# Optimization experiments

Hardware: AMD Instinct MI355X
Metric: run time of the kernel (lower is better)

Reference implementation:

```python
import jax, jax.numpy as jnp
import numpy as np
import math

B, S, HID, NH = 2, 2048, 1024, 16
HD = HID // NH  # head_dim = 64
TEMPERATURE = 1.0


def setup_inputs() -> dict:
    key = jax.random.key(0)
    ks = jax.random.split(key, 6)
    w = lambda k: (jax.random.normal(k, (HID, HID), dtype=jnp.float32) * 0.02)
    return {
        "hidden_states": jax.random.normal(ks[0], (B, S, HID), dtype=jnp.float32),
        "attention_mask": jnp.ones((B, S), dtype=jnp.float32),
        "Wq": w(ks[1]), "bq": jnp.zeros((HID,), jnp.float32),
        "Wk": w(ks[2]), "bk": jnp.zeros((HID,), jnp.float32),
        "Wv": w(ks[3]), "bv": jnp.zeros((HID,), jnp.float32),
        "Wo": w(ks[4]), "bo": jnp.zeros((HID,), jnp.float32),
    }


def reference(hidden_states, attention_mask, Wq, bq, Wk, bk, Wv, bv, Wo, bo):
    b, s, hid = hidden_states.shape
    heads = lambda x: x.reshape(b, s, NH, HD).transpose(0, 2, 1, 3)  # [b,h,s,d]

    q = heads(hidden_states @ Wq.T + bq)
    k = heads(hidden_states @ Wk.T + bk)
    v = heads(hidden_states @ Wv.T + bv)

    # padding mask applied multiplicatively to k and v
    m = attention_mask[:, None, :, None]  # [b,1,s,1]
    k = k * m
    v = v * m

    # auxiliary Hopfield state: k^T @ v per head -> [b,h,d,d]
    state = jnp.einsum("bhsd,bhse->bhde", k, v)

    # energy / scores
    energy = jnp.einsum("bhqd,bhkd->bhqk", q, k) / (TEMPERATURE * math.sqrt(HD))
    causal = jnp.triu(jnp.ones((s, s), dtype=bool), k=1)  # True above diagonal
    energy = jnp.where(causal[None, None], -jnp.inf, energy)
    energy = jnp.where(attention_mask[:, None, None, :] == 0, -jnp.inf, energy)

    attn = jax.nn.softmax(energy, axis=-1)
    out = jnp.einsum("bhqk,bhkd->bhqd", attn, v)
    out = out.transpose(0, 2, 1, 3).reshape(b, s, hid)
    out = out @ Wo.T + bo
    return out, state
```

## Files before the change

kernel.cpp:

```cpp
#include <hip/hip_runtime.h>
#include <hip/hip_bf16.h>

#define B_ 2
#define S_ 2048
#define HID_ 1024
#define NH_ 16
#define HD_ 64
#define MTOK (B_*S_)
#define LDQKV 3072

typedef __attribute__((ext_vector_type(8))) __bf16 bf16x8;
typedef __attribute__((ext_vector_type(4))) __bf16 bf16x4;
typedef __attribute__((ext_vector_type(4))) float f32x4;

__device__ __forceinline__ void gl16(__bf16* lds, const __bf16* g) {
  __builtin_amdgcn_global_load_lds(
      (const __attribute__((address_space(1))) void*)g,
      (__attribute__((address_space(3))) void*)lds, 16, 0, 0);
}
__device__ __forceinline__ void gl4(float* lds, const float* g) {
  __builtin_amdgcn_global_load_lds(
      (const __attribute__((address_space(1))) void*)g,
      (__attribute__((address_space(3))) void*)lds, 4, 0, 0);
}

__global__ __launch_bounds__(256) void cast_all(
    const float* __restrict__ X,
    const float* __restrict__ Wq, const float* __restrict__ Wk,
    const float* __restrict__ Wv, const float* __restrict__ Wo,
    __bf16* __restrict__ Xb, __bf16* __restrict__ Wqkvb, __bf16* __restrict__ Wob)
{
  int i = blockIdx.x * 256 + threadIdx.x;
  const float* src; __bf16* dst; int j;
  if (i < (1 << 20))              { src = X;  dst = Xb;                 j = i; }
  else if (i < (1<<20)+(1<<18))   { src = Wq; dst = Wqkvb;              j = i - (1<<20); }
  else if (i < (1<<20)+(2<<18))   { src = Wk; dst = Wqkvb + (1<<20);    j = i - (1<<20) - (1<<18); }
  else if (i < (1<<20)+(3<<18))   { src = Wv; dst = Wqkvb + (2<<20);    j = i - (1<<20) - (2<<18); }
  else                            { src = Wo; dst = Wob;                j = i - (1<<20) - (3<<18); }
  float4 v = reinterpret_cast<const float4*>(src)[j];
  bf16x4 o;
  o[0] = (__bf16)v.x; o[1] = (__bf16)v.y; o[2] = (__bf16)v.z; o[3] = (__bf16)v.w;
  reinterpret_cast<bf16x4*>(dst)[j] = o;
}

__global__ __launch_bounds__(256) void gemm_qkv(
    const __bf16* __restrict__ A, const __bf16* __restrict__ W,
    const float* __restrict__ bq, const float* __restrict__ bk,
    const float* __restrict__ bv, const float* __restrict__ mask,
    __bf16* __restrict__ C)
{
  __shared__ __bf16 As[2][128 * 32];
  __shared__ __bf16 Bs[2][128 * 32];
  const int t = threadIdx.x;
  const int m0 = blockIdx.y * 128;
  const int n0 = blockIdx.x * 128;
  const int lane = t & 63;
  const int w = t >> 6;
  const int wr = (w >> 1) * 64;
  const int wc = (w & 1) * 64;
  const int fr = lane & 15;
  const int kg = lane >> 4;

  f32x4 acc[4][4];
  #pragma unroll
  for (int i = 0; i < 4; i++)
    #pragma unroll
    for (int j = 0; j < 4; j++) acc[i][j] = (f32x4)0.f;

  const int srow = w * 16 + (lane >> 2);
  const int scol = (lane & 3) * 8;
  const __bf16* ap0 = A + (size_t)(m0 + srow) * HID_ + scol;
  const __bf16* ap1 = A + (size_t)(m0 + 64 + srow) * HID_ + scol;
  const __bf16* wp0 = W + (size_t)(n0 + srow) * HID_ + scol;
  const __bf16* wp1 = W + (size_t)(n0 + 64 + srow) * HID_ + scol;

  #define GSTAGE(buf, koff) \
    gl16(&As[buf][w * 512], ap0 + (koff)); \
    gl16(&As[buf][2048 + w * 512], ap1 + (koff)); \
    gl16(&Bs[buf][w * 512], wp0 + (koff)); \
    gl16(&Bs[buf][2048 + w * 512], wp1 + (koff));

  GSTAGE(0, 0);
  for (int k0 = 0; k0 < HID_; k0 += 32) {
    const int cur = (k0 >> 5) & 1;
    if (k0 + 32 < HID_) {
      GSTAGE(cur ^ 1, k0 + 32);
      asm volatile("s_waitcnt vmcnt(4)" ::: "memory");
    } else {
      asm volatile("s_waitcnt vmcnt(0)" ::: "memory");
    }
    __builtin_amdgcn_sched_barrier(0);
    __builtin_amdgcn_s_barrier();
    bf16x8 af[4], bf[4];
    #pragma unroll
    for (int m = 0; m < 4; m++) af[m] = *(const bf16x8*)&As[cur][(wr + m*16 + fr) * 32 + kg*8];
    #pragma unroll
    for (int n = 0; n < 4; n++) bf[n] = *(const bf16x8*)&Bs[cur][(wc + n*16 + fr) * 32 + kg*8];
    #pragma unroll
    for (int m = 0; m < 4; m++)
      #pragma unroll
      for (int n = 0; n < 4; n++)
        acc[m][n] = __builtin_amdgcn_mfma_f32_16x16x32_bf16(af[m], bf[n], acc[m][n], 0, 0, 0);
    __builtin_amdgcn_s_barrier();
  }

  const int region = n0 >> 10;
  const float* bias = region == 0 ? bq : (region == 1 ? bk : bv);
  const int nloc = n0 & 1023;

  #pragma unroll
  for (int m = 0; m < 4; m++) {
    #pragma unroll
    for (int r = 0; r < 4; r++) {
      int row = m0 + wr + m*16 + kg*4 + r;
      float rs = region ? mask[row] : 1.f;
      #pragma unroll
      for (int n = 0; n < 4; n++) {
        int c = wc + n*16 + fr;
        float v = (acc[m][n][r] + bias[nloc + c]) * rs;
        C[(size_t)row * LDQKV + n0 + c] = (__bf16)v;
      }
    }
  }
}

__global__ __launch_bounds__(256) void gemm_o(
    const __bf16* __restrict__ A, const __bf16* __restrict__ W,
    const float* __restrict__ bias, float* __restrict__ C)
{
  __shared__ __bf16 As[2][128 * 32];
  __shared__ __bf16 Bs[2][128 * 32];
  const int t = threadIdx.x;
  const int m0 = blockIdx.y * 128;
  const int n0 = blockIdx.x * 128;
  const int lane = t & 63;
  const int w = t >> 6;
  const int wr = (w >> 1) * 64;
  const int wc = (w & 1) * 64;
  const int fr = lane & 15;
  const int kg = lane >> 4;

  f32x4 acc[4][4];
  #pragma unroll
  for (int i = 0; i < 4; i++)
    #pragma unroll
    for (int j = 0; j < 4; j++) acc[i][j] = (f32x4)0.f;

  const int srow = w * 16 + (lane >> 2);
  const int scol = (lane & 3) * 8;
  const __bf16* ap0 = A + (size_t)(m0 + srow) * HID_ + scol;
  const __bf16* ap1 = A + (size_t)(m0 + 64 + srow) * HID_ + scol;
  const __bf16* wp0 = W + (size_t)(n0 + srow) * HID_ + scol;
  const __bf16* wp1 = W + (size_t)(n0 + 64 + srow) * HID_ + scol;

  GSTAGE(0, 0);
  for (int k0 = 0; k0 < HID_; k0 += 32) {
    const int cur = (k0 >> 5) & 1;
    if (k0 + 32 < HID_) {
      GSTAGE(cur ^ 1, k0 + 32);
      asm volatile("s_waitcnt vmcnt(4)" ::: "memory");
    } else {
      asm volatile("s_waitcnt vmcnt(0)" ::: "memory");
    }
    __builtin_amdgcn_sched_barrier(0);
    __builtin_amdgcn_s_barrier();
    bf16x8 af[4], bf[4];
    #pragma unroll
    for (int m = 0; m < 4; m++) af[m] = *(const bf16x8*)&As[cur][(wr + m*16 + fr) * 32 + kg*8];
    #pragma unroll
    for (int n = 0; n < 4; n++) bf[n] = *(const bf16x8*)&Bs[cur][(wc + n*16 + fr) * 32 + kg*8];
    #pragma unroll
    for (int m = 0; m < 4; m++)
      #pragma unroll
      for (int n = 0; n < 4; n++)
        acc[m][n] = __builtin_amdgcn_mfma_f32_16x16x32_bf16(af[m], bf[n], acc[m][n], 0, 0, 0);
    __builtin_amdgcn_s_barrier();
  }

  #pragma unroll
  for (int m = 0; m < 4; m++) {
    #pragma unroll
    for (int r = 0; r < 4; r++) {
      int row = m0 + wr + m*16 + kg*4 + r;
      #pragma unroll
      for (int n = 0; n < 4; n++) {
        int col = n0 + wc + n*16 + fr;
        C[(size_t)row * HID_ + col] = acc[m][n][r] + bias[col];
      }
    }
  }
}

__global__ __launch_bounds__(256) void transpose_kv(
    const __bf16* __restrict__ Kin, const __bf16* __restrict__ Vin,
    __bf16* __restrict__ Kt, __bf16* __restrict__ Vt)
{
  __shared__ __bf16 tile[64][68];
  const int tok0 = blockIdx.x * 64;
  const int f0 = blockIdx.y * 64;
  const __bf16* in = blockIdx.z ? Vin : Kin;
  __bf16* out = blockIdx.z ? Vt : Kt;
  const int t = threadIdx.x;
  const int r = t >> 2;
  const int c0 = (t & 3) * 16;
  const __bf16* src = in + (size_t)(tok0 + r) * LDQKV + f0 + c0;
  *(bf16x8*)&tile[r][c0]     = *(const bf16x8*)src;
  *(bf16x8*)&tile[r][c0 + 8] = *(const bf16x8*)(src + 8);
  __syncthreads();
  bf16x8 o0, o1;
  #pragma unroll
  for (int j = 0; j < 8; j++) { o0[j] = tile[c0 + j][r]; o1[j] = tile[c0 + 8 + j][r]; }
  __bf16* dst = out + (size_t)(f0 + r) * MTOK + tok0 + c0;
  *(bf16x8*)dst = o0;
  *(bf16x8*)(dst + 8) = o1;
}

#define SCALE_LOG2E 0.18033688011112043f

__device__ __forceinline__ bf16x8 ld_swz(const __bf16* base, int row, int xb) {
  return *(const bf16x8*)((const char*)base + row * 128 + (xb ^ ((row & 7) << 4)));
}
__device__ __forceinline__ void st_swz16(__bf16* base, int row, int colbyte, __bf16 v) {
  *(__bf16*)((char*)base + row * 128 + (colbyte ^ ((row & 7) << 4))) = v;
}
__device__ __forceinline__ bf16x8 ld_swz256(const __bf16* base, int row, int xb) {
  return *(const bf16x8*)((const char*)base + row * 256 + (xb ^ ((row & 7) << 4)));
}

__device__ __forceinline__ void attn_tile(
    const __bf16* __restrict__ ks, const __bf16* __restrict__ vs,
    const bool (&okm)[4], __bf16* __restrict__ pw,
    const bf16x8 (&qa)[2], f32x4 (&acc)[4], f32x4& accl,
    const bf16x8 ones, int q0w, int kt, int fc, int kg)
{
  f32x4 s[4];
  #pragma unroll
  for (int n = 0; n < 4; n++) s[n] = (f32x4)0.f;
  #pragma unroll
  for (int kd = 0; kd < 2; kd++)
    #pragma unroll
    for (int n = 0; n < 4; n++) {
      bf16x8 kf = ld_swz(ks, n * 16 + fc, kd * 64 + kg * 16);
      s[n] = __builtin_amdgcn_mfma_f32_16x16x32_bf16(qa[kd], kf, s[n], 0, 0, 0);
    }

  const int g4 = kg * 4;
  const bool fullt = (kt * 64 + 63 <= q0w);
  if (fullt) {
    #pragma unroll
    for (int r = 0; r < 4; r++)
      #pragma unroll
      for (int n = 0; n < 4; n++) {
        float p = okm[n] ? exp2f(s[n][r] * SCALE_LOG2E) : 0.f;
        st_swz16(pw, g4 + r, (n * 16 + fc) * 2, (__bf16)p);
      }
  } else {
    #pragma unroll
    for (int r = 0; r < 4; r++) {
      const int qg = q0w + g4 + r;
      #pragma unroll
      for (int n = 0; n < 4; n++) {
        bool ok = okm[n] && (kt * 64 + n * 16 + fc <= qg);
        float p = ok ? exp2f(s[n][r] * SCALE_LOG2E) : 0.f;
        st_swz16(pw, g4 + r, (n * 16 + fc) * 2, (__bf16)p);
      }
    }
  }

  #pragma unroll
  for (int kc = 0; kc < 2; kc++) {
    bf16x8 pf = ld_swz(pw, fc, kc * 64 + kg * 16);
    accl = __builtin_amdgcn_mfma_f32_16x16x32_bf16(pf, ones, accl, 0, 0, 0);
    #pragma unroll
    for (int n = 0; n < 4; n++) {
      bf16x8 vf = ld_swz(vs, n * 16 + fc, kc * 64 + kg * 16);
      acc[n] = __builtin_amdgcn_mfma_f32_16x16x32_bf16(pf, vf, acc[n], 0, 0, 0);
    }
  }
}

__global__ __launch_bounds__(256) void flash_mfma(
    const __bf16* __restrict__ Q, const __bf16* __restrict__ K,
    const __bf16* __restrict__ Vt, const float* __restrict__ mask,
    __bf16* __restrict__ O)
{
  __shared__ __bf16 Ks[2][64 * 64];
  __shared__ __bf16 Vs[2][64 * 64];
  __shared__ __bf16 Ps[4][16 * 64];
  __shared__ float mk[2][64];

  const int bh = blockIdx.x;
  const int qt = 31 - (int)blockIdx.y;
  const int b = bh >> 4, h = bh & 15;
  const int t = threadIdx.x;
  const int w = t >> 6;
  const int lane = t & 63;
  const int fc = lane & 15;
  const int kg = lane >> 4;
  const int g4 = kg * 4;

  const int q0w = qt * 64 + w * 16;
  const size_t tokbase = (size_t)b * S_;

  const int rr = lane >> 3;
  const int cswz = ((lane & 7) ^ rr) * 8;
  const int ktmax = qt;

  gl16(&Ks[0][(w * 16) * 64],     K + (tokbase + (size_t)(w * 16 + rr)) * LDQKV + h * HD_ + cswz);
  gl16(&Ks[0][(w * 16 + 8) * 64], K + (tokbase + (size_t)(w * 16 + 8 + rr)) * LDQKV + h * HD_ + cswz);
  gl16(&Vs[0][(w * 16) * 64],     Vt + (size_t)(h * HD_ + w * 16 + rr) * MTOK + tokbase + cswz);
  gl16(&Vs[0][(w * 16 + 8) * 64], Vt + (size_t)(h * HD_ + w * 16 + 8 + rr) * MTOK + tokbase + cswz);
  gl4(&mk[0][0], mask + tokbase + lane);

  bf16x8 qa[2];
  {
    const __bf16* qp = Q + (tokbase + q0w + fc) * LDQKV + h * HD_;
    qa[0] = *(const bf16x8*)(qp + kg * 8);
    qa[1] = *(const bf16x8*)(qp + 32 + kg * 8);
  }

  bf16x8 ones;
  #pragma unroll
  for (int j = 0; j < 8; j++) ones[j] = (__bf16)1.f;

  f32x4 acc[4], accl;
  #pragma unroll
  for (int n = 0; n < 4; n++) acc[n] = (f32x4)0.f;
  accl = (f32x4)0.f;

  __bf16* pw = &Ps[w][0];

  for (int kt = 0; kt <= ktmax; ++kt) {
    const int cur = kt & 1;
    if (kt < ktmax) {
      const int nxt = cur ^ 1;
      const size_t krow = tokbase + (size_t)((kt + 1) * 64);
      gl16(&Ks[nxt][(w * 16) * 64],     K + (krow + w * 16 + rr) * LDQKV + h * HD_ + cswz);
      gl16(&Ks[nxt][(w * 16 + 8) * 64], K + (krow + w * 16 + 8 + rr) * LDQKV + h * HD_ + cswz);
      gl16(&Vs[nxt][(w * 16) * 64],     Vt + (size_t)(h * HD_ + w * 16 + rr) * MTOK + tokbase + (kt + 1) * 64 + cswz);
      gl16(&Vs[nxt][(w * 16 + 8) * 64], Vt + (size_t)(h * HD_ + w * 16 + 8 + rr) * MTOK + tokbase + (kt + 1) * 64 + cswz);
      gl4(&mk[nxt][0], mask + tokbase + (kt + 1) * 64 + lane);
      asm volatile("s_waitcnt vmcnt(5)" ::: "memory");
    } else {
      asm volatile("s_waitcnt vmcnt(0)" ::: "memory");
    }
    __builtin_amdgcn_sched_barrier(0);
    __builtin_amdgcn_s_barrier();

    bool okm[4];
    #pragma unroll
    for (int n = 0; n < 4; n++) okm[n] = (mk[cur][n * 16 + fc] != 0.f);

    attn_tile(&Ks[cur][0], &Vs[cur][0], okm, pw, qa, acc, accl, ones, q0w, kt, fc, kg);

    __builtin_amdgcn_s_barrier();
  }

  #pragma unroll
  for (int r = 0; r < 4; r++) {
    float inv = accl[r] > 0.f ? 1.f / accl[r] : 0.f;
    __bf16* op = O + (tokbase + q0w + g4 + r) * HID_ + h * HD_;
    #pragma unroll
    for (int n = 0; n < 4; n++)
      op[n * 16 + fc] = (__bf16)(acc[n][r] * inv);
  }
}

__global__ __launch_bounds__(256) void state_mfma(
    const __bf16* __restrict__ Kt, const __bf16* __restrict__ Vt,
    float* __restrict__ part)
{
  __shared__ __bf16 Kl[64 * 128];
  __shared__ __bf16 Vl[64 * 128];
  const int bh = blockIdx.x, sc = blockIdx.y;
  const int b = bh >> 4, h = bh & 15;
  const int t = threadIdx.x;
  const int w = t >> 6;
  const int lane = t & 63;
  const int fc = lane & 15;
  const int kg = lane >> 4;
  const size_t colbase = (size_t)b * S_ + sc * 128;
  const int rloc = lane >> 4;
  const int cb = (lane & 15) * 16;

  #pragma unroll
  for (int c = 0; c < 4; c++) {
    int row = w * 16 + c * 4 + rloc;
    int scol = (cb ^ ((row & 7) << 4)) >> 1;
    gl16(&Kl[(w * 16 + c * 4) * 128], Kt + (size_t)(h * HD_ + row) * MTOK + colbase + scol);
    gl16(&Vl[(w * 16 + c * 4) * 128], Vt + (size_t)(h * HD_ + row) * MTOK + colbase + scol);
  }
  __syncthreads();

  f32x4 acc[4];
  #pragma unroll
  for (int n = 0; n < 4; n++) acc[n] = (f32x4)0.f;
  #pragma unroll
  for (int ks = 0; ks < 4; ks++) {
    bf16x8 af = ld_swz256(Kl, w * 16 + fc, ks * 64 + kg * 16);
    #pragma unroll
    for (int n = 0; n < 4; n++) {
      bf16x8 bfr = ld_swz256(Vl, n * 16 + fc, ks * 64 + kg * 16);
      acc[n] = __builtin_amdgcn_mfma_f32_16x16x32_bf16(af, bfr, acc[n], 0, 0, 0);
    }
  }

  float* dst = part + (((size_t)bh * 16 + sc) << 12);
  #pragma unroll
  for (int n = 0; n < 4; n++)
    #pragma unroll
    for (int r = 0; r < 4; r++)
      dst[(w * 16 + kg * 4 + r) * 64 + n * 16 + fc] = acc[n][r];
}

__global__ __launch_bounds__(256) void state_reduce(
    const float* __restrict__ part, float* __restrict__ out)
{
  int i = blockIdx.x * 256 + threadIdx.x;
  int bh = i >> 12, de = i & 4095;
  float s = 0.f;
  #pragma unroll
  for (int sc = 0; sc < 16; sc++) s += part[(((size_t)bh * 16 + sc) << 12) + de];
  out[i] = s;
}

extern "C" void kernel_launch(void* const* d_in, const int* in_sizes, int n_in,
                              void* d_out, int out_size, void* d_ws, size_t ws_size,
                              hipStream_t stream)
{
  const float* hs   = (const float*)d_in[0];
  const float* mask = (const float*)d_in[1];
  const float* Wq   = (const float*)d_in[2];
  const float* bq   = (const float*)d_in[3];
  const float* Wk   = (const float*)d_in[4];
  const float* bk   = (const float*)d_in[5];
  const float* Wv   = (const float*)d_in[6];
  const float* bv   = (const float*)d_in[7];
  const float* Wo   = (const float*)d_in[8];
  const float* bo   = (const float*)d_in[9];
  float* out = (float*)d_out;

  char* ws = (char*)d_ws;
  __bf16* Wqkvb = (__bf16*)(ws);
  __bf16* Wob   = (__bf16*)(ws + (6u  << 20));
  __bf16* Xb    = (__bf16*)(ws + (8u  << 20));
  __bf16* QKV   = (__bf16*)(ws + (16u << 20));
  __bf16* Ob    = (__bf16*)(ws + (40u << 20));
  __bf16* Ktg   = (__bf16*)(ws + (48u << 20));

  cast_all<<<8192, 256, 0, stream>>>(hs, Wq, Wk, Wv, Wo, Xb, Wqkvb, Wob);

  gemm_qkv<<<dim3(LDQKV / 128, MTOK / 128), 256, 0, stream>>>(
      Xb, Wqkvb, bq, bk, bv, mask, QKV);

  __bf16* Vtg = Xb;
  transpose_kv<<<dim3(MTOK / 64, HID_ / 64, 2), 256, 0, stream>>>(
      QKV + 1024, QKV + 2048, Ktg, Vtg);

  flash_mfma<<<dim3(B_ * NH_, 32), 256, 0, stream>>>(
      QKV, QKV + 1024, Vtg, mask, Ob);

  gemm_o<<<dim3(HID_ / 128, MTOK / 128), 256, 0, stream>>>(Ob, Wob, bo, out);

  float* part = (float*)Ob;
  state_mfma<<<dim3(B_ * NH_, 16), 256, 0, stream>>>(Ktg, Vtg, part);
  state_reduce<<<512, 256, 0, stream>>>(part, out + (size_t)MTOK * HID_);
}
```

Measured before the change: 140.9 us.

## Swizzle flash grid per XCD, keep mask in registers, use fast exp2

Flattens the flash-attention grid and remaps block ids so each XCD processes a contiguous set of heads, improving L2 reuse of K/V. The padding mask is loaded straight into registers instead of through LDS, and prefetch pointers are advanced incrementally. exp2f is replaced by the hardware exp2 builtin, trading some accuracy on denormals for fewer instructions. The wait count is adjusted for the changed load mix.

```diff
diff --git a/kernel.cpp b/kernel.cpp
--- a/kernel.cpp
+++ b/kernel.cpp
@@ -17,11 +17,6 @@
   __builtin_amdgcn_global_load_lds(
       (const __attribute__((address_space(1))) void*)g,
       (__attribute__((address_space(3))) void*)lds, 16, 0, 0);
-}
-__device__ __forceinline__ void gl4(float* lds, const float* g) {
-  __builtin_amdgcn_global_load_lds(
-      (const __attribute__((address_space(1))) void*)g,
-      (__attribute__((address_space(3))) void*)lds, 4, 0, 0);
 }
 
 __global__ __launch_bounds__(256) void cast_all(
@@ -251,7 +246,7 @@
     for (int r = 0; r < 4; r++)
       #pragma unroll
       for (int n = 0; n < 4; n++) {
-        float p = okm[n] ? exp2f(s[n][r] * SCALE_LOG2E) : 0.f;
+        float p = okm[n] ? __builtin_amdgcn_exp2f(s[n][r] * SCALE_LOG2E) : 0.f;
         st_swz16(pw, g4 + r, (n * 16 + fc) * 2, (__bf16)p);
       }
   } else {
@@ -261,7 +256,7 @@
       #pragma unroll
       for (int n = 0; n < 4; n++) {
         bool ok = okm[n] && (kt * 64 + n * 16 + fc <= qg);
-        float p = ok ? exp2f(s[n][r] * SCALE_LOG2E) : 0.f;
+        float p = ok ? __builtin_amdgcn_exp2f(s[n][r] * SCALE_LOG2E) : 0.f;
         st_swz16(pw, g4 + r, (n * 16 + fc) * 2, (__bf16)p);
       }
     }
@@ -287,10 +282,11 @@
   __shared__ __bf16 Ks[2][64 * 64];
   __shared__ __bf16 Vs[2][64 * 64];
   __shared__ __bf16 Ps[4][16 * 64];
-  __shared__ float mk[2][64];
-
-  const int bh = blockIdx.x;
-  const int qt = 31 - (int)blockIdx.y;
+
+  const int bid = blockIdx.x;
+  const int swz = (bid & 7) * 128 + (bid >> 3);
+  const int bh = swz >> 5;
+  const int qt = 31 - (swz & 31);
   const int b = bh >> 4, h = bh & 15;
   const int t = threadIdx.x;
   const int w = t >> 6;
@@ -306,12 +302,6 @@
   const int cswz = ((lane & 7) ^ rr) * 8;
   const int ktmax = qt;
 
-  gl16(&Ks[0][(w * 16) * 64],     K + (tokbase + (size_t)(w * 16 + rr)) * LDQKV + h * HD_ + cswz);
-  gl16(&Ks[0][(w * 16 + 8) * 64], K + (tokbase + (size_t)(w * 16 + 8 + rr)) * LDQKV + h * HD_ + cswz);
-  gl16(&Vs[0][(w * 16) * 64],     Vt + (size_t)(h * HD_ + w * 16 + rr) * MTOK + tokbase + cswz);
-  gl16(&Vs[0][(w * 16 + 8) * 64], Vt + (size_t)(h * HD_ + w * 16 + 8 + rr) * MTOK + tokbase + cswz);
-  gl4(&mk[0][0], mask + tokbase + lane);
-
   bf16x8 qa[2];
   {
     const __bf16* qp = Q + (tokbase + q0w + fc) * LDQKV + h * HD_;
@@ -319,6 +309,23 @@
     qa[1] = *(const bf16x8*)(qp + 32 + kg * 8);
   }
 
+  const float* mp = mask + tokbase + fc;
+  float mnxt[4];
+  #pragma unroll
+  for (int n = 0; n < 4; n++) mnxt[n] = mp[n * 16];
+
+  const __bf16* kp0 = K + (tokbase + (size_t)(w * 16 + rr)) * LDQKV + h * HD_ + cswz;
+  const __bf16* kp1 = kp0 + (size_t)8 * LDQKV;
+  const __bf16* vp0 = Vt + (size_t)(h * HD_ + w * 16 + rr) * MTOK + tokbase + cswz;
+  const __bf16* vp1 = vp0 + (size_t)8 * MTOK;
+
+  gl16(&Ks[0][(w * 16) * 64],     kp0);
+  gl16(&Ks[0][(w * 16 + 8) * 64], kp1);
+  gl16(&Vs[0][(w * 16) * 64],     vp0);
+  gl16(&Vs[0][(w * 16 + 8) * 64], vp1);
+  kp0 += (size_t)64 * LDQKV; kp1 += (size_t)64 * LDQKV;
+  vp0 += 64; vp1 += 64;
+
   bf16x8 ones;
   #pragma unroll
   for (int j = 0; j < 8; j++) ones[j] = (__bf16)1.f;
@@ -332,15 +339,21 @@
 
   for (int kt = 0; kt <= ktmax; ++kt) {
     const int cur = kt & 1;
+    float mcur[4];
+    #pragma unroll
+    for (int n = 0; n < 4; n++) mcur[n] = mnxt[n];
+
     if (kt < ktmax) {
+      #pragma unroll
+      for (int n = 0; n < 4; n++) mnxt[n] = mp[(kt + 1) * 64 + n * 16];
       const int nxt = cur ^ 1;
-      const size_t krow = tokbase + (size_t)((kt + 1) * 64);
-      gl16(&Ks[nxt][(w * 16) * 64],     K + (krow + w * 16 + rr) * LDQKV + h * HD_ + cswz);
-      gl16(&Ks[nxt][(w * 16 + 8) * 64], K + (krow + w * 16 + 8 + rr) * LDQKV + h * HD_ + cswz);
-      gl16(&Vs[nxt][(w * 16) * 64],     Vt + (size_t)(h * HD_ + w * 16 + rr) * MTOK + tokbase + (kt + 1) * 64 + cswz);
-      gl16(&Vs[nxt][(w * 16 + 8) * 64], Vt + (size_t)(h * HD_ + w * 16 + 8 + rr) * MTOK + tokbase + (kt + 1) * 64 + cswz);
-      gl4(&mk[nxt][0], mask + tokbase + (kt + 1) * 64 + lane);
-      asm volatile("s_waitcnt vmcnt(5)" ::: "memory");
+      gl16(&Ks[nxt][(w * 16) * 64],     kp0);
+      gl16(&Ks[nxt][(w * 16 + 8) * 64], kp1);
+      gl16(&Vs[nxt][(w * 16) * 64],     vp0);
+      gl16(&Vs[nxt][(w * 16 + 8) * 64], vp1);
+      kp0 += (size_t)64 * LDQKV; kp1 += (size_t)64 * LDQKV;
+      vp0 += 64; vp1 += 64;
+      asm volatile("s_waitcnt vmcnt(8)" ::: "memory");
     } else {
       asm volatile("s_waitcnt vmcnt(0)" ::: "memory");
     }
@@ -349,7 +362,7 @@
 
     bool okm[4];
     #pragma unroll
-    for (int n = 0; n < 4; n++) okm[n] = (mk[cur][n * 16 + fc] != 0.f);
+    for (int n = 0; n < 4; n++) okm[n] = (mcur[n] != 0.f);
 
     attn_tile(&Ks[cur][0], &Vs[cur][0], okm, pw, qa, acc, accl, ones, q0w, kt, fc, kg);
 
@@ -457,7 +470,7 @@
   transpose_kv<<<dim3(MTOK / 64, HID_ / 64, 2), 256, 0, stream>>>(
       QKV + 1024, QKV + 2048, Ktg, Vtg);
 
-  flash_mfma<<<dim3(B_ * NH_, 32), 256, 0, stream>>>(
+  flash_mfma<<<dim3(B_ * NH_ * 32), 256, 0, stream>>>(
       QKV, QKV + 1024, Vtg, mask, Ob);
 
   gemm_o<<<dim3(HID_ / 128, MTOK / 128), 256, 0, stream>>>(Ob, Wob, bo, out);
```

Measured after the change: 160.2 us. 1.14x slower.
